# Optimization experiments

Measured on AMD Instinct MI355X. Metric: run time of the kernel, lower is better.

## Reference

```python
import jax, jax.numpy as jnp
import numpy as np

B, N, DEG = 16, 2048, 16          # graphs, nodes per graph, avg out-degree
C_IN, HID, K = 64, 128, 32        # in_channels, hidden_channels, out_channels (clusters)
NT = B * N                        # total nodes
E = NT * DEG                      # total edges
GN_EPS = 1e-5


def setup_inputs() -> dict:
    key = jax.random.key(0)
    ks = jax.random.split(key, 6)
    x = jax.random.normal(ks[0], (NT, C_IN), jnp.float32)
    # within-graph random edges (sorted batch => node i belongs to graph i // N)
    src_l = jax.random.randint(ks[1], (E,), 0, N)
    dst_l = jax.random.randint(ks[2], (E,), 0, N)
    gid = jnp.repeat(jnp.arange(B, dtype=jnp.int32), N * DEG)
    edge_index = jnp.stack([gid * N + src_l, gid * N + dst_l]).astype(jnp.int32)
    batch = jnp.repeat(jnp.arange(B, dtype=jnp.int32), N)
    return dict(
        x=x, edge_index=edge_index, batch=batch,
        gn_weight=jnp.ones((C_IN,), jnp.float32),
        gn_bias=jnp.zeros((C_IN,), jnp.float32),
        gn_mean_scale=jnp.ones((C_IN,), jnp.float32),
        w1=jax.random.normal(ks[3], (C_IN, HID), jnp.float32) / np.float32(np.sqrt(C_IN)),
        b1=jnp.zeros((HID,), jnp.float32),
        w2=jax.random.normal(ks[4], (HID, K), jnp.float32) / np.float32(np.sqrt(HID)),
        b2=jnp.zeros((K,), jnp.float32),
    )


def reference(x, gn_weight, gn_bias, gn_mean_scale, w1, b1, w2, b2, edge_index, batch):
    # ---- GraphNorm (per-graph mean/var with learnable mean scale) ----
    ones_n = jnp.ones((NT,), x.dtype)
    cnt = jax.ops.segment_sum(ones_n, batch, num_segments=B)[:, None]        # [B,1]
    mean = jax.ops.segment_sum(x, batch, num_segments=B) / cnt              # [B,C]
    xm = x - gn_mean_scale * mean[batch]
    var = jax.ops.segment_sum(xm * xm, batch, num_segments=B) / cnt         # [B,C]
    h = gn_weight * xm / jnp.sqrt(var + GN_EPS)[batch] + gn_bias            # [NT,C_IN]

    # ---- GCNConv (add self-loops, symmetric D^-1/2 (A+I) D^-1/2) ----
    src, dst = edge_index[0], edge_index[1]
    loop = jnp.arange(NT, dtype=src.dtype)
    src_l = jnp.concatenate([src, loop])
    dst_l = jnp.concatenate([dst, loop])
    deg = jax.ops.segment_sum(jnp.ones_like(src_l, x.dtype), dst_l, num_segments=NT)
    dinv = jnp.where(deg > 0, jax.lax.rsqrt(deg), 0.0)
    norm = dinv[src_l] * dinv[dst_l]                                        # [E+NT]
    hw = h @ w1                                                             # [NT,HID]
    h = jax.ops.segment_sum(norm[:, None] * hw[src_l], dst_l, num_segments=NT) + b1
    h = jax.nn.selu(h)

    # ---- to_dense_batch / to_dense_adj (uniform graph sizes -> mask all True) ----
    xd = h.reshape(B, N, HID)                                               # [B,N,F]
    adj = jnp.zeros((B, N, N), x.dtype).at[batch[src], src % N, dst % N].add(1.0)

    # ---- DMoNPooling ----
    s = jax.nn.softmax(xd @ w2 + b2, axis=-1)                               # [B,N,K]
    out = jax.nn.selu(jnp.einsum('bnk,bnf->bkf', s, xd))                    # [B,K,F]
    sta = jnp.einsum('bnk,bnm->bkm', s, adj)                                # [B,K,N]
    out_adj = jnp.einsum('bkm,bml->bkl', sta, s)                            # [B,K,K]

    degrees = adj.sum(-1)                                                   # [B,N]
    m = degrees.sum(-1) / 2                                                 # [B]
    ca = jnp.einsum('bnk,bn->bk', s, degrees)                               # [B,K]
    normalizer = ca[:, :, None] * ca[:, None, :] / 2 / m[:, None, None]
    spectral_loss = (-jnp.einsum('bkk->b', out_adj - normalizer) / (2 * m)).mean()

    ss = jnp.einsum('bnk,bnl->bkl', s, s)                                   # [B,K,K]
    ss_fro = jnp.sqrt(jnp.sum(ss * ss, axis=(-2, -1), keepdims=True))
    eye = jnp.eye(K, dtype=x.dtype)
    diff = ss / ss_fro - eye / jnp.sqrt(jnp.float32(K))
    ortho_loss = jnp.sqrt(jnp.sum(diff * diff, axis=(-2, -1))).mean()

    cluster_size = s.sum(1)                                                 # [B,K]
    cluster_loss = (jnp.linalg.norm(cluster_size, axis=1) / N
                    * jnp.sqrt(jnp.float32(K)) - 1).mean()
    # (coarsened-adj renormalization in DMoNPooling is unused by Net's outputs)

    return jax.nn.log_softmax(out, axis=-1), spectral_loss + ortho_loss + cluster_loss, s
```

## Files before the change

kernel.cpp:

```cpp
#include <hip/hip_runtime.h>
#include <cmath>

static constexpr int B_  = 16;
static constexpr int N_  = 2048;
static constexpr int NT_ = 32768;
static constexpr int E_  = 524288;

static constexpr size_t OFF_HSC    = 0;
static constexpr size_t OFF_XD     = 2097152;
static constexpr size_t OFF_SWS    = 6291456;
static constexpr size_t OFF_PART   = 7340032;
static constexpr size_t OFF_GSP    = 9437184;
static constexpr size_t OFF_GSP2   = 9445376;
static constexpr size_t OFF_SSP    = 9453568;
static constexpr size_t OFF_CAP    = 9977856;
static constexpr size_t OFF_CSP    = 9994240;
static constexpr size_t OFF_IHIN   = 10043904;
static constexpr size_t OFF_IHOUT  = 10306048;
static constexpr size_t OFF_IROWS  = 10830336;
static constexpr size_t OFF_IESRC  = 10895876;

__device__ __forceinline__ float selu_f(float x) {
  return 1.0507009873554805f * (x > 0.f ? x : 1.6732632423543772f * expm1f(x));
}

__device__ __forceinline__ float block_sum_bcast(float v, float* sm) {
  int lane = threadIdx.x & 63, w = threadIdx.x >> 6;
#pragma unroll
  for (int off = 32; off; off >>= 1) v += __shfl_down(v, off);
  __syncthreads();
  if (lane == 0) sm[w] = v;
  __syncthreads();
  return sm[0] + sm[1] + sm[2] + sm[3];
}

__global__ __launch_bounds__(1024) void k_count(const int* ei, const float* x,
                                                int* histin, int* histout,
                                                float* gsp, float* gsp2) {
  __shared__ int hin[2048], hout[2048];
  __shared__ float l1[16][64], l2[16][64];
  int blk = blockIdx.x;
  int tid = threadIdx.x;
  if (blk < 128) {
    int g = blk >> 3, p = blk & 7;
    int nbase = g * 2048, ebase = g * 32768 + p * 4096;
    hin[tid] = 0; hin[tid + 1024] = 0;
    hout[tid] = 0; hout[tid + 1024] = 0;
    __syncthreads();
#pragma unroll
    for (int it = 0; it < 4; it++) {
      int e = ebase + it * 1024 + tid;
      int s = ei[e], d = ei[E_ + e];
      atomicAdd(&hout[s - nbase], 1);
      atomicAdd(&hin[d - nbase], 1);
    }
    __syncthreads();
    histin[blk * 2048 + tid] = hin[tid];
    histin[blk * 2048 + tid + 1024] = hin[tid + 1024];
    histout[blk * 2048 + tid] = hout[tid];
    histout[blk * 2048 + tid + 1024] = hout[tid + 1024];
  } else {
    int gi = blk - 128;
    int b = gi >> 3, chunk = gi & 7;
    int c = tid & 63, r = tid >> 6;
    float s = 0.f, s2 = 0.f;
    const float* xb = x + ((size_t)b * N_ + (size_t)chunk * 256) * 64;
    for (int n = r; n < 256; n += 16) {
      float v = xb[n * 64 + c];
      s += v; s2 += v * v;
    }
    l1[r][c] = s; l2[r][c] = s2;
    __syncthreads();
    if (r == 0) {
      float t1 = 0.f, t2 = 0.f;
#pragma unroll
      for (int i = 0; i < 16; i++) { t1 += l1[i][c]; t2 += l2[i][c]; }
      gsp[gi * 64 + c] = t1;
      gsp2[gi * 64 + c] = t2;
    }
  }
}

__global__ __launch_bounds__(256) void k_prepb(const float* x, const float* gsp,
                                               const float* gsp2, const float* gw,
                                               const float* gb, const float* gms,
                                               float* hsc, const int* ei,
                                               const int* histin, int* rows,
                                               int* esrc) {
  int tid = threadIdx.x;
  int blk = blockIdx.x;
  if (blk < 128) {
    __shared__ int tot[2048], cur[2048];
    __shared__ int wsum[4];
    int g = blk >> 3, p = blk & 7;
    int nbase = g * 2048, ebase = g * 32768;
    for (int i = tid; i < 2048; i += 256) { tot[i] = 0; cur[i] = 0; }
    __syncthreads();
    for (int q = 0; q < 8; q++) {
      const int* hq = &histin[(g * 8 + q) * 2048];
      for (int i = tid; i < 2048; i += 256) {
        int v = hq[i];
        tot[i] += v;
        if (q < p) cur[i] += v;
      }
    }
    __syncthreads();
    int base = tid * 8;
    int loc[8]; int run = 0;
#pragma unroll
    for (int j = 0; j < 8; j++) { loc[j] = run; run += tot[base + j]; }
    int lane = tid & 63, w = tid >> 6;
    int incl = run;
#pragma unroll
    for (int off = 1; off < 64; off <<= 1) {
      int t = __shfl_up(incl, off);
      if (lane >= off) incl += t;
    }
    if (lane == 63) wsum[w] = incl;
    __syncthreads();
    int woffv = 0;
    for (int k = 0; k < w; k++) woffv += wsum[k];
    int texcl = incl - run + woffv;
#pragma unroll
    for (int j = 0; j < 8; j++) {
      int pre = cur[base + j];
      int rv = ebase + texcl + loc[j];
      if (p == 0) rows[nbase + base + j] = rv;
      cur[base + j] = rv + pre;
    }
    if (p == 0 && g == 15 && tid == 255) rows[NT_] = E_;
    __syncthreads();
    int ebp = ebase + p * 4096;
#pragma unroll
    for (int it = 0; it < 16; it++) {
      int e = ebp + it * 256 + tid;
      int s = ei[e], d = ei[E_ + e];
      int pos = atomicAdd(&cur[d - nbase], 1);
      esrc[pos] = s;
    }
  } else {
    __shared__ float shs[64], scs[64], sdin[16];
    int bb = blk - 128;
    int bgr = bb >> 7;
    int nl = (bb & 127) * 16;
    if (tid < 128) {
      int node16 = tid >> 3, q = tid & 7;
      int v = histin[(bgr * 8 + q) * 2048 + nl + node16];
      v += __shfl_down(v, 4, 8);
      v += __shfl_down(v, 2, 8);
      v += __shfl_down(v, 1, 8);
      if (q == 0) sdin[node16] = rsqrtf((float)(v + 1));
    }
    if (tid < 64) {
      float s = 0.f, s2 = 0.f;
#pragma unroll
      for (int c8 = 0; c8 < 8; c8++) {
        s  += gsp[(bgr * 8 + c8) * 64 + tid];
        s2 += gsp2[(bgr * 8 + c8) * 64 + tid];
      }
      float mean = s * (1.f / 2048.f);
      float a = gms[tid];
      float var = s2 * (1.f / 2048.f) - (2.f * a - a * a) * mean * mean;
      shs[tid] = a * mean;
      scs[tid] = gw[tid] * rsqrtf(var + 1e-5f);
    }
    __syncthreads();
    int idx = bb * 256 + tid;
    int node = idx >> 4, g4 = (idx & 15) * 4;
    float di = sdin[tid >> 4];
    float4 xv = *(const float4*)&x[(size_t)node * 64 + g4];
    float4 bbv = *(const float4*)&gb[g4];
    float4 o;
    o.x = ((xv.x - shs[g4])     * scs[g4]     + bbv.x) * di;
    o.y = ((xv.y - shs[g4 + 1]) * scs[g4 + 1] + bbv.y) * di;
    o.z = ((xv.z - shs[g4 + 2]) * scs[g4 + 2] + bbv.z) * di;
    o.w = ((xv.w - shs[g4 + 3]) * scs[g4 + 3] + bbv.w) * di;
    *(float4*)&hsc[(size_t)node * 64 + g4] = o;
  }
}

__global__ __launch_bounds__(256, 8) void k_mm1(const float* hsc, const int* rows,
                                                const int* esrc, const float* w1,
                                                const float* b1, float* xd) {
  __shared__ float at[32 * 65];
  int tid = threadIdx.x;
  int bid = blockIdx.x;
  int xcd = bid & 7, slot = bid >> 3;
  int g = xcd + ((slot >> 6) << 3);
  int n0 = g * 2048 + (slot & 63) * 32;
  int wv = tid >> 6, c = tid & 63;
#pragma unroll 1
  for (int i = 0; i < 8; i++) {
    int nn = i * 4 + wv;
    int node = n0 + nn;
    int e0 = rows[node], e1 = rows[node + 1];
    float dd = rsqrtf((float)(e1 - e0 + 1));
    float acc = hsc[(size_t)node * 64 + c];
    for (int e = e0; e < e1; e += 8) {
      int sidx[8]; float wt[8], hv[8];
#pragma unroll
      for (int j = 0; j < 8; j++) {
        int ee = e + j;
        sidx[j] = esrc[ee < e1 ? ee : e0];
        wt[j] = (ee < e1) ? 1.f : 0.f;
      }
#pragma unroll
      for (int j = 0; j < 8; j++) hv[j] = hsc[(size_t)sidx[j] * 64 + c];
#pragma unroll
      for (int j = 0; j < 8; j++) acc += wt[j] * hv[j];
    }
    at[nn * 65 + c] = dd * acc;
  }
  __syncthreads();
  int tx = tid & 31, ty = tid >> 5;
  int f0 = tx * 4, nn = ty * 4;
  float acc[4][4] = {};
  for (int k = 0; k < 64; k++) {
    float4 wvv = *(const float4*)&w1[k * 128 + f0];
#pragma unroll
    for (int i = 0; i < 4; i++) {
      float av = at[(nn + i) * 65 + k];
      acc[i][0] += av * wvv.x; acc[i][1] += av * wvv.y;
      acc[i][2] += av * wvv.z; acc[i][3] += av * wvv.w;
    }
  }
  float4 bv = *(const float4*)&b1[f0];
#pragma unroll
  for (int i = 0; i < 4; i++) {
    float4 o;
    o.x = selu_f(acc[i][0] + bv.x);
    o.y = selu_f(acc[i][1] + bv.y);
    o.z = selu_f(acc[i][2] + bv.z);
    o.w = selu_f(acc[i][3] + bv.w);
    *(float4*)&xd[(size_t)(n0 + nn + i) * 128 + f0] = o;
  }
}

__global__ __launch_bounds__(256) void k_mm2f(const float* xd, const float* w2,
                                              const float* b2, const int* histout,
                                              float* outs, float* ssp,
                                              float* cap, float* csp, float* part) {
  __shared__ float xt[64 * 129];
  __shared__ float st[64 * 33];
  __shared__ float r1[8][32], r2[8][32];
  __shared__ float cdeg[64];
  int tid = threadIdx.x;
  int blk = blockIdx.x;
  int n0 = blk * 64;
  int g = n0 >> 11, nl0 = n0 & 2047;
  if (tid < 64) {
    int ssum = 0;
#pragma unroll
    for (int q = 0; q < 8; q++) ssum += histout[(g * 8 + q) * 2048 + nl0 + tid];
    cdeg[tid] = (float)ssum;
  }
  for (int i = tid; i < 2048; i += 256) {
    int n = i >> 5, j4 = (i & 31) * 4;
    float4 v = *(const float4*)&xd[(size_t)(n0 + n) * 128 + j4];
    xt[n * 129 + j4] = v.x; xt[n * 129 + j4 + 1] = v.y;
    xt[n * 129 + j4 + 2] = v.z; xt[n * 129 + j4 + 3] = v.w;
  }
  __syncthreads();
  int ty = tid >> 3;
  int k0 = (tid & 7) * 4;
  float acc2[2][4] = {};
  for (int j = 0; j < 128; j++) {
    float4 wv = *(const float4*)&w2[j * 32 + k0];
    float x0 = xt[(ty * 2) * 129 + j];
    float x1 = xt[(ty * 2 + 1) * 129 + j];
    acc2[0][0] += x0 * wv.x; acc2[0][1] += x0 * wv.y; acc2[0][2] += x0 * wv.z; acc2[0][3] += x0 * wv.w;
    acc2[1][0] += x1 * wv.x; acc2[1][1] += x1 * wv.y; acc2[1][2] += x1 * wv.z; acc2[1][3] += x1 * wv.w;
  }
  float4 bv2 = *(const float4*)&b2[k0];
#pragma unroll
  for (int i = 0; i < 2; i++) {
    int n = ty * 2 + i;
    st[n * 33 + k0]     = acc2[i][0] + bv2.x;
    st[n * 33 + k0 + 1] = acc2[i][1] + bv2.y;
    st[n * 33 + k0 + 2] = acc2[i][2] + bv2.z;
    st[n * 33 + k0 + 3] = acc2[i][3] + bv2.w;
  }
  __syncthreads();
  {
    int n = tid >> 2, q = (tid & 3) * 8;
    float m = -3.4e38f;
#pragma unroll
    for (int j = 0; j < 8; j++) m = fmaxf(m, st[n * 33 + q + j]);
#pragma unroll
    for (int off = 1; off < 4; off <<= 1) m = fmaxf(m, __shfl_xor(m, off, 4));
    float ev[8]; float ssum = 0.f;
#pragma unroll
    for (int j = 0; j < 8; j++) { ev[j] = expf(st[n * 33 + q + j] - m); ssum += ev[j]; }
#pragma unroll
    for (int off = 1; off < 4; off <<= 1) ssum += __shfl_xor(ssum, off, 4);
    float inv = 1.f / ssum;
#pragma unroll
    for (int j = 0; j < 8; j++) st[n * 33 + q + j] = ev[j] * inv;
  }
  __syncthreads();
  for (int i = tid; i < 512; i += 256) {
    int n = i >> 3, q = (i & 7) * 4;
    float* op = &outs[(size_t)(n0 + n) * 32 + q];
    op[0] = st[n * 33 + q];
    op[1] = st[n * 33 + q + 1];
    op[2] = st[n * 33 + q + 2];
    op[3] = st[n * 33 + q + 3];
  }
  {
    int k = tid >> 3, l0 = (tid & 7) * 4;
    float a0 = 0, a1 = 0, a2 = 0, a3 = 0;
    for (int n = 0; n < 64; n++) {
      float sk = st[n * 33 + k];
      a0 += sk * st[n * 33 + l0];     a1 += sk * st[n * 33 + l0 + 1];
      a2 += sk * st[n * 33 + l0 + 2]; a3 += sk * st[n * 33 + l0 + 3];
    }
    float4 o = {a0, a1, a2, a3};
    *(float4*)&ssp[(size_t)blk * 1024 + k * 32 + l0] = o;
  }
  {
    int k2 = tid & 31, r = tid >> 5;
    float aca = 0.f, acs = 0.f;
    for (int i = 0; i < 8; i++) {
      int n = i * 8 + r;
      float dg = cdeg[n];
      float v = st[n * 33 + k2];
      acs += v; aca += v * dg;
    }
    r1[r][k2] = aca; r2[r][k2] = acs;
    __syncthreads();
    if (r == 0) {
      float sa = 0.f, sc = 0.f;
#pragma unroll
      for (int i = 0; i < 8; i++) { sa += r1[i][k2]; sc += r2[i][k2]; }
      cap[blk * 32 + k2] = sa;
      csp[blk * 32 + k2] = sc;
    }
  }
  {
    int tx = tid & 31, ty2 = tid >> 5;
    int f0 = tx * 4, kk0 = ty2 * 4;
    float acc[4][4] = {};
    for (int n = 0; n < 64; n++) {
      float s0 = st[n * 33 + kk0], s1 = st[n * 33 + kk0 + 1];
      float s2 = st[n * 33 + kk0 + 2], s3 = st[n * 33 + kk0 + 3];
      float4 xv = {xt[n * 129 + f0], xt[n * 129 + f0 + 1], xt[n * 129 + f0 + 2], xt[n * 129 + f0 + 3]};
      acc[0][0] += s0 * xv.x; acc[0][1] += s0 * xv.y; acc[0][2] += s0 * xv.z; acc[0][3] += s0 * xv.w;
      acc[1][0] += s1 * xv.x; acc[1][1] += s1 * xv.y; acc[1][2] += s1 * xv.z; acc[1][3] += s1 * xv.w;
      acc[2][0] += s2 * xv.x; acc[2][1] += s2 * xv.y; acc[2][2] += s2 * xv.z; acc[2][3] += s2 * xv.w;
      acc[3][0] += s3 * xv.x; acc[3][1] += s3 * xv.y; acc[3][2] += s3 * xv.z; acc[3][3] += s3 * xv.w;
    }
#pragma unroll
    for (int i = 0; i < 4; i++) {
      float4 o = {acc[i][0], acc[i][1], acc[i][2], acc[i][3]};
      *(float4*)&part[(size_t)(blk * 32 + kk0 + i) * 128 + f0] = o;
    }
  }
}

__global__ __launch_bounds__(256) void k_spec2(const int* rows, const int* esrc,
                                               const float* s, const float* part,
                                               float* specp, float* out0,
                                               float* lossp) {
  __shared__ float smem[8];
  int blk = blockIdx.x, tid = threadIdx.x;
  if (blk == 0 && tid == 0) lossp[0] = 0.f;
  if (blk < 1024) {
    int xcd = blk & 7, slot = blk >> 3;
    int g = xcd + ((slot >> 6) << 3);
    int grp = tid >> 5, k = tid & 31;
    int n0 = g * 2048 + (slot & 63) * 32 + grp * 4;
    float acc = 0.f;
#pragma unroll 1
    for (int i = 0; i < 4; i++) {
      int node = n0 + i;
      int e0 = rows[node], e1 = rows[node + 1];
      float sd = s[(size_t)node * 32 + k];
      float agg = 0.f;
      for (int e = e0; e < e1; e += 8) {
        int si[8]; float wt[8], sv[8];
#pragma unroll
        for (int j = 0; j < 8; j++) {
          int ee = e + j;
          si[j] = esrc[ee < e1 ? ee : e0];
          wt[j] = (ee < e1) ? 1.f : 0.f;
        }
#pragma unroll
        for (int j = 0; j < 8; j++) sv[j] = s[(size_t)si[j] * 32 + k];
#pragma unroll
        for (int j = 0; j < 8; j++) agg += wt[j] * sv[j];
      }
      acc += sd * agg;
    }
#pragma unroll
    for (int off = 16; off; off >>= 1) acc += __shfl_down(acc, off, 32);
    if (k == 0) smem[grp] = acc;
    __syncthreads();
    if (tid == 0) {
      specp[blk] = smem[0] + smem[1] + smem[2] + smem[3]
                 + smem[4] + smem[5] + smem[6] + smem[7];
    }
  } else {
    int rb = blk - 1024;
    int half = tid >> 7;
    int f = tid & 127;
    int row = rb * 2 + half;
    int b = row >> 5, k = row & 31;
    float v = 0.f;
#pragma unroll
    for (int c = 0; c < 32; c++) v += part[(size_t)((b * 32 + c) * 32 + k) * 128 + f];
    v = selu_f(v);
    int lane = tid & 63, w = tid >> 6;
    float m = v;
#pragma unroll
    for (int off = 32; off; off >>= 1) m = fmaxf(m, __shfl_down(m, off));
    if (lane == 0) smem[w] = m;
    __syncthreads();
    m = fmaxf(smem[half * 2], smem[half * 2 + 1]);
    float e = expf(v - m);
    float t = e;
    __syncthreads();
#pragma unroll
    for (int off = 32; off; off >>= 1) t += __shfl_down(t, off);
    if (lane == 0) smem[w] = t;
    __syncthreads();
    float tot = smem[half * 2] + smem[half * 2 + 1];
    out0[(size_t)row * 128 + f] = v - m - logf(tot);
  }
}

__global__ __launch_bounds__(256) void k_fin2(const float* ssp, const float* csp,
                                              const float* cap, const float* specp,
                                              float* loss) {
  __shared__ float sred[4];
  int b = blockIdx.x;
  int tid = threadIdx.x;
  float v0 = 0, v1 = 0, v2 = 0, v3 = 0;
  for (int c = 0; c < 32; c++) {
    float4 u = *(const float4*)&ssp[(size_t)(b * 32 + c) * 1024 + tid * 4];
    v0 += u.x; v1 += u.y; v2 += u.z; v3 += u.w;
  }
  float ssq = v0 * v0 + v1 * v1 + v2 * v2 + v3 * v3;
  ssq = block_sum_bcast(ssq, sred);
  float inv = 1.f / sqrtf(ssq);
  float dsq = 0.f;
  {
    int i0 = tid * 4;
    float vv[4] = {v0, v1, v2, v3};
#pragma unroll
    for (int jj = 0; jj < 4; jj++) {
      int i = i0 + jj;
      float d = vv[jj] * inv;
      if ((i >> 5) == (i & 31)) d -= 0.17677669529663687f;
      dsq += d * d;
    }
  }
  dsq = block_sum_bcast(dsq, sred);
  float csq = 0.f, casq = 0.f;
  if (tid < 32) {
    float c1 = 0.f, c2 = 0.f;
    for (int c = 0; c < 32; c++) {
      c1 += csp[(size_t)(b * 32 + c) * 32 + tid];
      c2 += cap[(size_t)(b * 32 + c) * 32 + tid];
    }
    csq = c1 * c1; casq = c2 * c2;
  }
  csq = block_sum_bcast(csq, sred);
  casq = block_sum_bcast(casq, sred);
  float spec_sum = 0.f;
  if (tid < 64) spec_sum = specp[(b & 7) + 8 * ((b >> 3) * 64 + tid)];
  spec_sum = block_sum_bcast(spec_sum, sred);
  if (tid == 0) {
    float ortho = sqrtf(dsq);
    float cl = sqrtf(csq) * (1.f / 2048.f) * 5.656854249492381f - 1.f;
    float m = 16384.f;
    float spec = -(spec_sum - casq / (2.f * m)) / (2.f * m);
    atomicAdd(loss, (spec + ortho + cl) * (1.f / 16.f));
  }
}

extern "C" void kernel_launch(void* const* d_in, const int* in_sizes, int n_in,
                              void* d_out, int out_size, void* d_ws, size_t ws_size,
                              hipStream_t stream) {
  (void)in_sizes; (void)n_in; (void)out_size; (void)ws_size;
  const float* x   = (const float*)d_in[0];
  const int*   ei  = (const int*)d_in[1];
  const float* gw  = (const float*)d_in[3];
  const float* gb  = (const float*)d_in[4];
  const float* gms = (const float*)d_in[5];
  const float* w1  = (const float*)d_in[6];
  const float* b1  = (const float*)d_in[7];
  const float* w2  = (const float*)d_in[8];
  const float* b2  = (const float*)d_in[9];
  float* out = (float*)d_out;
  float* ws  = (float*)d_ws;

  float* hsc    = ws + OFF_HSC;
  float* xd     = ws + OFF_XD;
  float* part   = ws + OFF_PART;
  float* gsp    = ws + OFF_GSP;
  float* gsp2   = ws + OFF_GSP2;
  float* ssp    = ws + OFF_SSP;
  float* cap    = ws + OFF_CAP;
  float* csp    = ws + OFF_CSP;
  float* specp  = ws + OFF_SWS;
  int*   histin = (int*)(ws + OFF_IHIN);
  int*   histout= (int*)(ws + OFF_IHOUT);
  int*   rows   = (int*)(ws + OFF_IROWS);
  int*   esrc   = (int*)(ws + OFF_IESRC);

  float* out0  = out;
  float* lossp = out + 65536;
  float* outs  = out + 65537;

  hipLaunchKernelGGL(k_count, dim3(256), dim3(1024), 0, stream, ei, x, histin, histout, gsp, gsp2);
  hipLaunchKernelGGL(k_prepb, dim3(2176), dim3(256), 0, stream,
                     x, gsp, gsp2, gw, gb, gms, hsc, ei, histin, rows, esrc);
  hipLaunchKernelGGL(k_mm1, dim3(1024), dim3(256), 0, stream, hsc, rows, esrc, w1, b1, xd);
  hipLaunchKernelGGL(k_mm2f, dim3(512), dim3(256), 0, stream,
                     xd, w2, b2, histout, outs, ssp, cap, csp, part);
  hipLaunchKernelGGL(k_spec2, dim3(1280), dim3(256), 0, stream,
                     rows, esrc, outs, part, specp, out0, lossp);
  hipLaunchKernelGGL(k_fin2, dim3(16), dim3(256), 0, stream,
                     ssp, csp, cap, specp, lossp);
}
```

Measured before the change: 183.0 us.

## Fuse GCN aggregation and first linear layer into the second matmul kernel

Merges k_mm1 into k_mm2f so each 64-node tile gathers neighbor features, applies W1+SELU into shared memory, and proceeds straight to the W2/DMoN reductions. This drops the xd intermediate write and read (16 MB round trip) and one kernel launch. Blocks are remapped to an XCD-aware graph/tile order with outputs indexed by logical tile. The trade-off is half as many blocks (512 instead of 1024 for the gather phase) and more registers per thread (8x4 accumulators), which may reduce occupancy and latency hiding for the irregular gather.

```diff
diff --git a/kernel.cpp b/kernel.cpp
--- a/kernel.cpp
+++ b/kernel.cpp
@@ -7,7 +7,6 @@
 static constexpr int E_  = 524288;
 
 static constexpr size_t OFF_HSC    = 0;
-static constexpr size_t OFF_XD     = 2097152;
 static constexpr size_t OFF_SWS    = 6291456;
 static constexpr size_t OFF_PART   = 7340032;
 static constexpr size_t OFF_GSP    = 9437184;
@@ -179,64 +178,9 @@
   }
 }
 
-__global__ __launch_bounds__(256, 8) void k_mm1(const float* hsc, const int* rows,
-                                                const int* esrc, const float* w1,
-                                                const float* b1, float* xd) {
-  __shared__ float at[32 * 65];
-  int tid = threadIdx.x;
-  int bid = blockIdx.x;
-  int xcd = bid & 7, slot = bid >> 3;
-  int g = xcd + ((slot >> 6) << 3);
-  int n0 = g * 2048 + (slot & 63) * 32;
-  int wv = tid >> 6, c = tid & 63;
-#pragma unroll 1
-  for (int i = 0; i < 8; i++) {
-    int nn = i * 4 + wv;
-    int node = n0 + nn;
-    int e0 = rows[node], e1 = rows[node + 1];
-    float dd = rsqrtf((float)(e1 - e0 + 1));
-    float acc = hsc[(size_t)node * 64 + c];
-    for (int e = e0; e < e1; e += 8) {
-      int sidx[8]; float wt[8], hv[8];
-#pragma unroll
-      for (int j = 0; j < 8; j++) {
-        int ee = e + j;
-        sidx[j] = esrc[ee < e1 ? ee : e0];
-        wt[j] = (ee < e1) ? 1.f : 0.f;
-      }
-#pragma unroll
-      for (int j = 0; j < 8; j++) hv[j] = hsc[(size_t)sidx[j] * 64 + c];
-#pragma unroll
-      for (int j = 0; j < 8; j++) acc += wt[j] * hv[j];
-    }
-    at[nn * 65 + c] = dd * acc;
-  }
-  __syncthreads();
-  int tx = tid & 31, ty = tid >> 5;
-  int f0 = tx * 4, nn = ty * 4;
-  float acc[4][4] = {};
-  for (int k = 0; k < 64; k++) {
-    float4 wvv = *(const float4*)&w1[k * 128 + f0];
-#pragma unroll
-    for (int i = 0; i < 4; i++) {
-      float av = at[(nn + i) * 65 + k];
-      acc[i][0] += av * wvv.x; acc[i][1] += av * wvv.y;
-      acc[i][2] += av * wvv.z; acc[i][3] += av * wvv.w;
-    }
-  }
-  float4 bv = *(const float4*)&b1[f0];
-#pragma unroll
-  for (int i = 0; i < 4; i++) {
-    float4 o;
-    o.x = selu_f(acc[i][0] + bv.x);
-    o.y = selu_f(acc[i][1] + bv.y);
-    o.z = selu_f(acc[i][2] + bv.z);
-    o.w = selu_f(acc[i][3] + bv.w);
-    *(float4*)&xd[(size_t)(n0 + nn + i) * 128 + f0] = o;
-  }
-}
-
-__global__ __launch_bounds__(256) void k_mm2f(const float* xd, const float* w2,
+__global__ __launch_bounds__(256) void k_mm2g(const float* hsc, const int* rows,
+                                              const int* esrc, const float* w1,
+                                              const float* b1, const float* w2,
                                               const float* b2, const int* histout,
                                               float* outs, float* ssp,
                                               float* cap, float* csp, float* part) {
@@ -244,21 +188,70 @@
   __shared__ float st[64 * 33];
   __shared__ float r1[8][32], r2[8][32];
   __shared__ float cdeg[64];
+  float* at = xt;
   int tid = threadIdx.x;
   int blk = blockIdx.x;
-  int n0 = blk * 64;
-  int g = n0 >> 11, nl0 = n0 & 2047;
+  int xcd = blk & 7, slot = blk >> 3;
+  int g = xcd + ((slot >> 5) << 3);
+  int tile = slot & 31;
+  int lt = g * 32 + tile;
+  int n0 = g * 2048 + tile * 64;
+  int nl0 = tile * 64;
   if (tid < 64) {
     int ssum = 0;
 #pragma unroll
     for (int q = 0; q < 8; q++) ssum += histout[(g * 8 + q) * 2048 + nl0 + tid];
     cdeg[tid] = (float)ssum;
   }
-  for (int i = tid; i < 2048; i += 256) {
-    int n = i >> 5, j4 = (i & 31) * 4;
-    float4 v = *(const float4*)&xd[(size_t)(n0 + n) * 128 + j4];
-    xt[n * 129 + j4] = v.x; xt[n * 129 + j4 + 1] = v.y;
-    xt[n * 129 + j4 + 2] = v.z; xt[n * 129 + j4 + 3] = v.w;
+  {
+    int wv = tid >> 6, c = tid & 63;
+#pragma unroll 1
+    for (int i = 0; i < 16; i++) {
+      int nn = i * 4 + wv;
+      int node = n0 + nn;
+      int e0 = rows[node], e1 = rows[node + 1];
+      float dd = rsqrtf((float)(e1 - e0 + 1));
+      float acc = hsc[(size_t)node * 64 + c];
+      for (int e = e0; e < e1; e += 8) {
+        int sidx[8]; float wt[8], hv[8];
+#pragma unroll
+        for (int j = 0; j < 8; j++) {
+          int ee = e + j;
+          sidx[j] = esrc[ee < e1 ? ee : e0];
+          wt[j] = (ee < e1) ? 1.f : 0.f;
+        }
+#pragma unroll
+        for (int j = 0; j < 8; j++) hv[j] = hsc[(size_t)sidx[j] * 64 + c];
+#pragma unroll
+        for (int j = 0; j < 8; j++) acc += wt[j] * hv[j];
+      }
+      at[nn * 65 + c] = dd * acc;
+    }
+  }
+  __syncthreads();
+  {
+    int tx = tid & 31, ty = tid >> 5;
+    int f0 = tx * 4;
+    float a1[8][4] = {};
+    for (int k = 0; k < 64; k++) {
+      float4 wvv = *(const float4*)&w1[k * 128 + f0];
+#pragma unroll
+      for (int i = 0; i < 8; i++) {
+        float av = at[(ty * 8 + i) * 65 + k];
+        a1[i][0] += av * wvv.x; a1[i][1] += av * wvv.y;
+        a1[i][2] += av * wvv.z; a1[i][3] += av * wvv.w;
+      }
+    }
+    float4 b1v = *(const float4*)&b1[f0];
+    __syncthreads();
+#pragma unroll
+    for (int i = 0; i < 8; i++) {
+      int n = ty * 8 + i;
+      xt[n * 129 + f0]     = selu_f(a1[i][0] + b1v.x);
+      xt[n * 129 + f0 + 1] = selu_f(a1[i][1] + b1v.y);
+      xt[n * 129 + f0 + 2] = selu_f(a1[i][2] + b1v.z);
+      xt[n * 129 + f0 + 3] = selu_f(a1[i][3] + b1v.w);
+    }
   }
   __syncthreads();
   int ty = tid >> 3;
@@ -315,7 +308,7 @@
       a2 += sk * st[n * 33 + l0 + 2]; a3 += sk * st[n * 33 + l0 + 3];
     }
     float4 o = {a0, a1, a2, a3};
-    *(float4*)&ssp[(size_t)blk * 1024 + k * 32 + l0] = o;
+    *(float4*)&ssp[(size_t)lt * 1024 + k * 32 + l0] = o;
   }
   {
     int k2 = tid & 31, r = tid >> 5;
@@ -332,8 +325,8 @@
       float sa = 0.f, sc = 0.f;
 #pragma unroll
       for (int i = 0; i < 8; i++) { sa += r1[i][k2]; sc += r2[i][k2]; }
-      cap[blk * 32 + k2] = sa;
-      csp[blk * 32 + k2] = sc;
+      cap[lt * 32 + k2] = sa;
+      csp[lt * 32 + k2] = sc;
     }
   }
   {
@@ -352,7 +345,7 @@
 #pragma unroll
     for (int i = 0; i < 4; i++) {
       float4 o = {acc[i][0], acc[i][1], acc[i][2], acc[i][3]};
-      *(float4*)&part[(size_t)(blk * 32 + kk0 + i) * 128 + f0] = o;
+      *(float4*)&part[(size_t)(lt * 32 + kk0 + i) * 128 + f0] = o;
     }
   }
 }
@@ -495,7 +488,6 @@
   float* ws  = (float*)d_ws;
 
   float* hsc    = ws + OFF_HSC;
-  float* xd     = ws + OFF_XD;
   float* part   = ws + OFF_PART;
   float* gsp    = ws + OFF_GSP;
   float* gsp2   = ws + OFF_GSP2;
@@ -515,9 +507,9 @@
   hipLaunchKernelGGL(k_count, dim3(256), dim3(1024), 0, stream, ei, x, histin, histout, gsp, gsp2);
   hipLaunchKernelGGL(k_prepb, dim3(2176), dim3(256), 0, stream,
                      x, gsp, gsp2, gw, gb, gms, hsc, ei, histin, rows, esrc);
-  hipLaunchKernelGGL(k_mm1, dim3(1024), dim3(256), 0, stream, hsc, rows, esrc, w1, b1, xd);
-  hipLaunchKernelGGL(k_mm2f, dim3(512), dim3(256), 0, stream,
-                     xd, w2, b2, histout, outs, ssp, cap, csp, part);
+  hipLaunchKernelGGL(k_mm2g, dim3(512), dim3(256), 0, stream,
+                     hsc, rows, esrc, w1, b1, w2, b2, histout,
+                     outs, ssp, cap, csp, part);
   hipLaunchKernelGGL(k_spec2, dim3(1280), dim3(256), 0, stream,
                      rows, esrc, outs, part, specp, out0, lossp);
   hipLaunchKernelGGL(k_fin2, dim3(16), dim3(256), 0, stream,
```

After: 183.9 us. Within noise of the previous version (+0.5%).
